# Performance work log

Hardware: AMD Instinct MI355X
Metric: run time of the kernel (lower is better)

Reference implementation:

```python
import jax, jax.numpy as jnp
import numpy as np

B, S, D_IN, D_OUT = 4, 2048, 4096, 11008


def setup_inputs() -> dict:
    key = jax.random.key(0)
    k1, k2, k3 = jax.random.split(key, 3)
    x = jax.random.normal(k1, (B, S, D_IN), dtype=jnp.float32)
    # int8-range quantized weight values in [-127, 127]
    weight_q = jax.random.randint(k2, (D_OUT, D_IN), -127, 128, dtype=jnp.int32)
    # per-output-row abs-max scale (positive)
    max_val = jax.random.uniform(k3, (D_OUT,), dtype=jnp.float32, minval=0.5, maxval=4.0)
    return {"x": x, "weight_q": weight_q, "max_val": max_val}


def reference(x, weight_q, max_val):
    # dequantize: W = weight_q * max_val[:, None] / 127   (shape [D_OUT, D_IN])
    w = weight_q.astype(x.dtype) * (max_val / 127.0)[:, None]
    # F.linear(x, W) = x @ W.T
    return jnp.einsum('bsd,od->bso', x, w)
```

## Files before the change

### kernel.cpp

```cpp
#include <hip/hip_runtime.h>
#include <hip/hip_bf16.h>
#include <stdint.h>

constexpr int Mdim = 4 * 2048;
constexpr int Kdim = 4096;
constexpr int Ndim = 11008;

constexpr int BM = 128;
constexpr int BN = 128;
constexpr int BK = 32;

typedef _Float16 f16x8 __attribute__((ext_vector_type(8)));
typedef _Float16 f16x4 __attribute__((ext_vector_type(4)));
typedef float    f32x4 __attribute__((ext_vector_type(4)));
typedef int      i32x4 __attribute__((ext_vector_type(4)));


__global__ __launch_bounds__(256) void cvt_f32_f16(const float* __restrict__ in,
                                                   _Float16* __restrict__ out,
                                                   int nvec8) {
  int idx = blockIdx.x * blockDim.x + threadIdx.x;
  int stride = gridDim.x * blockDim.x;
  for (int i = idx; i < nvec8; i += stride) {
    const f32x4* p = (const f32x4*)in + (size_t)i * 2;
    f32x4 a = p[0];
    f32x4 b = p[1];
    f16x8 h;
    h[0] = (_Float16)a[0]; h[1] = (_Float16)a[1];
    h[2] = (_Float16)a[2]; h[3] = (_Float16)a[3];
    h[4] = (_Float16)b[0]; h[5] = (_Float16)b[1];
    h[6] = (_Float16)b[2]; h[7] = (_Float16)b[3];
    ((f16x8*)out)[i] = h;
  }
}

__global__ __launch_bounds__(256) void cvt_i32_f16(const int* __restrict__ in,
                                                   _Float16* __restrict__ out,
                                                   int nvec8) {
  int idx = blockIdx.x * blockDim.x + threadIdx.x;
  int stride = gridDim.x * blockDim.x;
  for (int i = idx; i < nvec8; i += stride) {
    const i32x4* p = (const i32x4*)in + (size_t)i * 2;
    i32x4 a = p[0];
    i32x4 b = p[1];
    f16x8 h;
    h[0] = (_Float16)a[0]; h[1] = (_Float16)a[1];
    h[2] = (_Float16)a[2]; h[3] = (_Float16)a[3];
    h[4] = (_Float16)b[0]; h[5] = (_Float16)b[1];
    h[6] = (_Float16)b[2]; h[7] = (_Float16)b[3];
    ((f16x8*)out)[i] = h;
  }
}


__device__ __forceinline__ void gl_lds16(const _Float16* g, _Float16* l) {
  __builtin_amdgcn_global_load_lds(
      (const __attribute__((address_space(1))) unsigned int*)g,
      (__attribute__((address_space(3))) unsigned int*)l,
      16, 0, 0);
}


template <bool FROM_WS>
__global__ __launch_bounds__(256) void w8_gemm(const void* __restrict__ Ap,
                                               const void* __restrict__ Bp,
                                               const float* __restrict__ maxval,
                                               float* __restrict__ C) {
  __shared__ _Float16 As[BM][BK];
  __shared__ _Float16 Bs[BN][BK];

  const int nbn = Ndim / BN;
  const int nwg = (Mdim / BM) * nbn;
  const int cpx = nwg / 8;
  int bid = blockIdx.x;
  bid = (bid % 8) * cpx + (bid / 8);
  const int bm = bid / nbn;
  const int bn = bid % nbn;
  const int rowBase = bm * BM;
  const int colBase = bn * BN;

  const int t = threadIdx.x;
  const int lane = t & 63;
  const int wid = t >> 6;
  const int wr = wid >> 1;
  const int wc = wid & 1;
  const int lrow = lane & 15;
  const int kgrp = lane >> 4;

  f32x4 acc[4][4] = {};

  for (int k0 = 0; k0 < Kdim; k0 += BK) {
    __syncthreads();
    if constexpr (FROM_WS) {
      const _Float16* A  = (const _Float16*)Ap;
      const _Float16* Bw = (const _Float16*)Bp;
#pragma unroll
      for (int i = 0; i < 2; ++i) {
        int c = i * 256 + t;
        int r = c >> 2;
        int ce = (c & 3) * 8;
        gl_lds16(A  + (size_t)(rowBase + r) * Kdim + k0 + ce, &As[r][ce]);
        gl_lds16(Bw + (size_t)(colBase + r) * Kdim + k0 + ce, &Bs[r][ce]);
      }
    } else {
      const float* A  = (const float*)Ap;
      const int*   Bw = (const int*)Bp;
#pragma unroll
      for (int i = 0; i < 4; ++i) {
        int c = i * 256 + t;
        int r = c >> 3;
        int ce = (c & 7) * 4;
        f32x4 av = *(const f32x4*)(A  + (size_t)(rowBase + r) * Kdim + k0 + ce);
        i32x4 bv = *(const i32x4*)(Bw + (size_t)(colBase + r) * Kdim + k0 + ce);
        f16x4 ah, bh;
#pragma unroll
        for (int j = 0; j < 4; ++j) {
          ah[j] = (_Float16)av[j];
          bh[j] = (_Float16)bv[j];
        }
        *(f16x4*)&As[r][ce] = ah;
        *(f16x4*)&Bs[r][ce] = bh;
      }
    }
    __syncthreads();

    f16x8 a[4], b[4];
#pragma unroll
    for (int m = 0; m < 4; ++m)
      a[m] = *(const f16x8*)&As[wr * 64 + m * 16 + lrow][kgrp * 8];
#pragma unroll
    for (int n = 0; n < 4; ++n)
      b[n] = *(const f16x8*)&Bs[wc * 64 + n * 16 + lrow][kgrp * 8];
#pragma unroll
    for (int m = 0; m < 4; ++m)
#pragma unroll
      for (int n = 0; n < 4; ++n)
        acc[m][n] = __builtin_amdgcn_mfma_f32_16x16x32_f16(a[m], b[n], acc[m][n], 0, 0, 0);
  }

  float s[4];
#pragma unroll
  for (int n = 0; n < 4; ++n)
    s[n] = maxval[colBase + wc * 64 + n * 16 + lrow] * (1.0f / 127.0f);
#pragma unroll
  for (int m = 0; m < 4; ++m) {
#pragma unroll
    for (int j = 0; j < 4; ++j) {
      int row = rowBase + wr * 64 + m * 16 + kgrp * 4 + j;
      float* cp = C + (size_t)row * Ndim + colBase + wc * 64 + lrow;
#pragma unroll
      for (int n = 0; n < 4; ++n)
        cp[n * 16] = acc[m][n][j] * s[n];
    }
  }
}


extern "C" void kernel_launch(void* const* d_in, const int* in_sizes, int n_in,
                              void* d_out, int out_size, void* d_ws, size_t ws_size,
                              hipStream_t stream) {
  const float* x  = (const float*)d_in[0];
  const int*   wq = (const int*)d_in[1];
  const float* mx = (const float*)d_in[2];
  float* out = (float*)d_out;

  const size_t xh_bytes = (size_t)Mdim * Kdim * sizeof(_Float16);
  const size_t wh_bytes = (size_t)Ndim * Kdim * sizeof(_Float16);
  const int nblocks = (Mdim / BM) * (Ndim / BN);

  if (ws_size >= xh_bytes + wh_bytes) {
    _Float16* xh = (_Float16*)d_ws;
    _Float16* wh = (_Float16*)((char*)d_ws + xh_bytes);
    cvt_f32_f16<<<2048, 256, 0, stream>>>(x, xh, Mdim * Kdim / 8);
    cvt_i32_f16<<<2048, 256, 0, stream>>>(wq, wh, Ndim * Kdim / 8);
    w8_gemm<true><<<nblocks, 256, 0, stream>>>(xh, wh, mx, out);
  } else {
    w8_gemm<false><<<nblocks, 256, 0, stream>>>(x, wq, mx, out);
  }
}
```

Before: 1.461 ms.

## Use 256x256 tiles with triple-buffered swizzled LDS pipeline in fp16 GEMM

```diff
diff --git a/kernel.cpp b/kernel.cpp
--- a/kernel.cpp
+++ b/kernel.cpp
@@ -2,13 +2,9 @@
 #include <hip/hip_bf16.h>
 #include <stdint.h>
 
-constexpr int Mdim = 4 * 2048;
+constexpr int Mdim = 8192;
 constexpr int Kdim = 4096;
 constexpr int Ndim = 11008;
-
-constexpr int BM = 128;
-constexpr int BN = 128;
-constexpr int BK = 32;
 
 typedef _Float16 f16x8 __attribute__((ext_vector_type(8)));
 typedef _Float16 f16x4 __attribute__((ext_vector_type(4)));
@@ -60,99 +56,187 @@
       16, 0, 0);
 }
 
-
-template <bool FROM_WS>
-__global__ __launch_bounds__(256) void w8_gemm(const void* __restrict__ Ap,
-                                               const void* __restrict__ Bp,
-                                               const float* __restrict__ maxval,
-                                               float* __restrict__ C) {
-  __shared__ _Float16 As[BM][BK];
-  __shared__ _Float16 Bs[BN][BK];
+#define WAITV4()    asm volatile("s_waitcnt vmcnt(4)" ::: "memory")
+#define WAITV0()    asm volatile("s_waitcnt vmcnt(0)" ::: "memory")
+#define WAITLGKM0() asm volatile("s_waitcnt lgkmcnt(0)" ::: "memory")
+#define SBAR()      __builtin_amdgcn_s_barrier()
+#define SCHED0()    __builtin_amdgcn_sched_barrier(0)
+#define MFMA16(d, va, vb) d = __builtin_amdgcn_mfma_f32_16x16x32_f16(va, vb, d, 0, 0, 0)
+
+
+constexpr int BM = 256, BN = 256, BK = 32;
+constexpr int NT = Kdim / BK;
+
+__global__ __launch_bounds__(512, 2) void w8_gemm256(
+    const _Float16* __restrict__ A, const _Float16* __restrict__ Bw,
+    const float* __restrict__ maxval, float* __restrict__ C) {
+  __shared__ _Float16 As[3][BM][BK];
+  __shared__ _Float16 Bs[3][BM][BK];
 
   const int nbn = Ndim / BN;
-  const int nwg = (Mdim / BM) * nbn;
-  const int cpx = nwg / 8;
+  const int cpx = ((Mdim / BM) * nbn) / 8;
   int bid = blockIdx.x;
-  bid = (bid % 8) * cpx + (bid / 8);
-  const int bm = bid / nbn;
-  const int bn = bid % nbn;
-  const int rowBase = bm * BM;
-  const int colBase = bn * BN;
+  bid = (bid & 7) * cpx + (bid >> 3);
+  const int rowBase = (bid / nbn) * BM;
+  const int colBase = (bid % nbn) * BN;
 
   const int t = threadIdx.x;
   const int lane = t & 63;
   const int wid = t >> 6;
-  const int wr = wid >> 1;
-  const int wc = wid & 1;
+  const int wr = wid >> 2;
+  const int wc = wid & 3;
   const int lrow = lane & 15;
   const int kgrp = lane >> 4;
 
+  const int sr = t >> 2;
+  const int sc = ((t & 3) ^ ((sr >> 2) & 3)) << 3;
+  const size_t aRow0 = (size_t)(rowBase + sr) * Kdim + sc;
+  const size_t aRow1 = (size_t)(rowBase + 128 + sr) * Kdim + sc;
+  const size_t bRow0 = (size_t)(colBase + sr) * Kdim + sc;
+  const size_t bRow1 = (size_t)(colBase + 128 + sr) * Kdim + sc;
+  const int ldsOff = t * 8;
+
+#define STAGE_A(buf, k0) do { \
+    gl_lds16(A + aRow0 + (k0), (_Float16*)As[buf] + ldsOff); \
+    gl_lds16(A + aRow1 + (k0), (_Float16*)As[buf] + 4096 + ldsOff); } while (0)
+#define STAGE_B(buf, k0) do { \
+    gl_lds16(Bw + bRow0 + (k0), (_Float16*)Bs[buf] + ldsOff); \
+    gl_lds16(Bw + bRow1 + (k0), (_Float16*)Bs[buf] + 4096 + ldsOff); } while (0)
+
+  int offA[8], offB[4];
+#pragma unroll
+  for (int m = 0; m < 8; ++m) {
+    int rt = wr * 128 + m * 16 + lrow;
+    offA[m] = rt * 64 + ((kgrp ^ ((rt >> 2) & 3)) << 4);
+  }
+#pragma unroll
+  for (int n = 0; n < 4; ++n) {
+    int rt = wc * 64 + n * 16 + lrow;
+    offB[n] = rt * 64 + ((kgrp ^ ((rt >> 2) & 3)) << 4);
+  }
+
+#define RDA(buf, m) (*(const f16x8*)((const char*)&As[buf][0][0] + offA[m]))
+#define RDB(buf, n) (*(const f16x8*)((const char*)&Bs[buf][0][0] + offB[n]))
+
+  f32x4 acc[8][4] = {};
+
+  STAGE_A(0, 0); STAGE_B(0, 0);
+  STAGE_A(1, BK); STAGE_B(1, BK);
+  WAITV4();
+  SBAR();
+
+  int cur = 0, nx1 = 1, nx2 = 2;
+  for (int T = 0; T < NT; ++T) {
+    const int kst = (T + 2) * BK;
+    if (T + 2 < NT) STAGE_A(nx2, kst);
+    f16x8 a0 = RDA(cur, 0), a1 = RDA(cur, 1), a2 = RDA(cur, 2), a3 = RDA(cur, 3);
+    f16x8 b0 = RDB(cur, 0), b1 = RDB(cur, 1), b2 = RDB(cur, 2), b3 = RDB(cur, 3);
+    SBAR();
+    WAITLGKM0();
+    SCHED0();
+    __builtin_amdgcn_s_setprio(1);
+    MFMA16(acc[0][0], a0, b0); MFMA16(acc[0][1], a0, b1); MFMA16(acc[0][2], a0, b2); MFMA16(acc[0][3], a0, b3);
+    MFMA16(acc[1][0], a1, b0); MFMA16(acc[1][1], a1, b1); MFMA16(acc[1][2], a1, b2); MFMA16(acc[1][3], a1, b3);
+    MFMA16(acc[2][0], a2, b0); MFMA16(acc[2][1], a2, b1); MFMA16(acc[2][2], a2, b2); MFMA16(acc[2][3], a2, b3);
+    MFMA16(acc[3][0], a3, b0); MFMA16(acc[3][1], a3, b1); MFMA16(acc[3][2], a3, b2); MFMA16(acc[3][3], a3, b3);
+    __builtin_amdgcn_s_setprio(0);
+    SBAR();
+    if (T + 2 < NT) STAGE_B(nx2, kst);
+    f16x8 a4 = RDA(cur, 4), a5 = RDA(cur, 5), a6 = RDA(cur, 6), a7 = RDA(cur, 7);
+    SBAR();
+    WAITLGKM0();
+    SCHED0();
+    __builtin_amdgcn_s_setprio(1);
+    MFMA16(acc[4][0], a4, b0); MFMA16(acc[4][1], a4, b1); MFMA16(acc[4][2], a4, b2); MFMA16(acc[4][3], a4, b3);
+    MFMA16(acc[5][0], a5, b0); MFMA16(acc[5][1], a5, b1); MFMA16(acc[5][2], a5, b2); MFMA16(acc[5][3], a5, b3);
+    MFMA16(acc[6][0], a6, b0); MFMA16(acc[6][1], a6, b1); MFMA16(acc[6][2], a6, b2); MFMA16(acc[6][3], a6, b3);
+    MFMA16(acc[7][0], a7, b0); MFMA16(acc[7][1], a7, b1); MFMA16(acc[7][2], a7, b2); MFMA16(acc[7][3], a7, b3);
+    __builtin_amdgcn_s_setprio(0);
+    if (T < NT - 2) { WAITV4(); } else { WAITV0(); }
+    SBAR();
+    int tmp = cur; cur = nx1; nx1 = nx2; nx2 = tmp;
+  }
+
+  float s[4];
+#pragma unroll
+  for (int n = 0; n < 4; ++n)
+    s[n] = maxval[colBase + wc * 64 + n * 16 + lrow] * (1.0f / 127.0f);
+#pragma unroll
+  for (int m = 0; m < 8; ++m) {
+#pragma unroll
+    for (int j = 0; j < 4; ++j) {
+      int row = rowBase + wr * 128 + m * 16 + kgrp * 4 + j;
+      float* cp = C + (size_t)row * Ndim + colBase + wc * 64 + lrow;
+#pragma unroll
+      for (int n = 0; n < 4; ++n)
+        cp[n * 16] = acc[m][n][j] * s[n];
+    }
+  }
+#undef STAGE_A
+#undef STAGE_B
+#undef RDA
+#undef RDB
+}
+
+
+__global__ __launch_bounds__(256) void w8_gemm_fb(const float* __restrict__ A,
+                                                  const int* __restrict__ Bw,
+                                                  const float* __restrict__ maxval,
+                                                  float* __restrict__ C) {
+  __shared__ _Float16 Asb[128][32];
+  __shared__ _Float16 Bsb[128][32];
+  const int nbn = Ndim / 128;
+  const int cpx = ((Mdim / 128) * nbn) / 8;
+  int bid = blockIdx.x;
+  bid = (bid & 7) * cpx + (bid >> 3);
+  const int rowBase = (bid / nbn) * 128;
+  const int colBase = (bid % nbn) * 128;
+  const int t = threadIdx.x;
+  const int lane = t & 63;
+  const int wid = t >> 6;
+  const int wr = wid >> 1, wc = wid & 1;
+  const int lrow = lane & 15, kgrp = lane >> 4;
   f32x4 acc[4][4] = {};
-
-  for (int k0 = 0; k0 < Kdim; k0 += BK) {
+  for (int k0 = 0; k0 < Kdim; k0 += 32) {
     __syncthreads();
-    if constexpr (FROM_WS) {
-      const _Float16* A  = (const _Float16*)Ap;
-      const _Float16* Bw = (const _Float16*)Bp;
-#pragma unroll
-      for (int i = 0; i < 2; ++i) {
-        int c = i * 256 + t;
-        int r = c >> 2;
-        int ce = (c & 3) * 8;
-        gl_lds16(A  + (size_t)(rowBase + r) * Kdim + k0 + ce, &As[r][ce]);
-        gl_lds16(Bw + (size_t)(colBase + r) * Kdim + k0 + ce, &Bs[r][ce]);
-      }
-    } else {
-      const float* A  = (const float*)Ap;
-      const int*   Bw = (const int*)Bp;
-#pragma unroll
-      for (int i = 0; i < 4; ++i) {
-        int c = i * 256 + t;
-        int r = c >> 3;
-        int ce = (c & 7) * 4;
-        f32x4 av = *(const f32x4*)(A  + (size_t)(rowBase + r) * Kdim + k0 + ce);
-        i32x4 bv = *(const i32x4*)(Bw + (size_t)(colBase + r) * Kdim + k0 + ce);
-        f16x4 ah, bh;
-#pragma unroll
-        for (int j = 0; j < 4; ++j) {
-          ah[j] = (_Float16)av[j];
-          bh[j] = (_Float16)bv[j];
-        }
-        *(f16x4*)&As[r][ce] = ah;
-        *(f16x4*)&Bs[r][ce] = bh;
-      }
+#pragma unroll
+    for (int i = 0; i < 4; ++i) {
+      int c = i * 256 + t;
+      int r = c >> 3;
+      int ce = (c & 7) * 4;
+      f32x4 av = *(const f32x4*)(A + (size_t)(rowBase + r) * Kdim + k0 + ce);
+      i32x4 bv = *(const i32x4*)(Bw + (size_t)(colBase + r) * Kdim + k0 + ce);
+      f16x4 ah, bh;
+#pragma unroll
+      for (int j = 0; j < 4; ++j) { ah[j] = (_Float16)av[j]; bh[j] = (_Float16)bv[j]; }
+      *(f16x4*)&Asb[r][ce] = ah;
+      *(f16x4*)&Bsb[r][ce] = bh;
     }
     __syncthreads();
-
     f16x8 a[4], b[4];
 #pragma unroll
-    for (int m = 0; m < 4; ++m)
-      a[m] = *(const f16x8*)&As[wr * 64 + m * 16 + lrow][kgrp * 8];
-#pragma unroll
-    for (int n = 0; n < 4; ++n)
-      b[n] = *(const f16x8*)&Bs[wc * 64 + n * 16 + lrow][kgrp * 8];
+    for (int m = 0; m < 4; ++m) a[m] = *(const f16x8*)&Asb[wr * 64 + m * 16 + lrow][kgrp * 8];
+#pragma unroll
+    for (int n = 0; n < 4; ++n) b[n] = *(const f16x8*)&Bsb[wc * 64 + n * 16 + lrow][kgrp * 8];
 #pragma unroll
     for (int m = 0; m < 4; ++m)
 #pragma unroll
       for (int n = 0; n < 4; ++n)
         acc[m][n] = __builtin_amdgcn_mfma_f32_16x16x32_f16(a[m], b[n], acc[m][n], 0, 0, 0);
   }
-
   float s[4];
 #pragma unroll
   for (int n = 0; n < 4; ++n)
     s[n] = maxval[colBase + wc * 64 + n * 16 + lrow] * (1.0f / 127.0f);
 #pragma unroll
-  for (int m = 0; m < 4; ++m) {
+  for (int m = 0; m < 4; ++m)
 #pragma unroll
     for (int j = 0; j < 4; ++j) {
       int row = rowBase + wr * 64 + m * 16 + kgrp * 4 + j;
       float* cp = C + (size_t)row * Ndim + colBase + wc * 64 + lrow;
 #pragma unroll
-      for (int n = 0; n < 4; ++n)
-        cp[n * 16] = acc[m][n][j] * s[n];
+      for (int n = 0; n < 4; ++n) cp[n * 16] = acc[m][n][j] * s[n];
     }
-  }
 }
 
 
@@ -166,15 +250,16 @@
 
   const size_t xh_bytes = (size_t)Mdim * Kdim * sizeof(_Float16);
   const size_t wh_bytes = (size_t)Ndim * Kdim * sizeof(_Float16);
-  const int nblocks = (Mdim / BM) * (Ndim / BN);
 
   if (ws_size >= xh_bytes + wh_bytes) {
     _Float16* xh = (_Float16*)d_ws;
     _Float16* wh = (_Float16*)((char*)d_ws + xh_bytes);
     cvt_f32_f16<<<2048, 256, 0, stream>>>(x, xh, Mdim * Kdim / 8);
     cvt_i32_f16<<<2048, 256, 0, stream>>>(wq, wh, Ndim * Kdim / 8);
-    w8_gemm<true><<<nblocks, 256, 0, stream>>>(xh, wh, mx, out);
+    const int nblocks = (Mdim / BM) * (Ndim / BN);
+    w8_gemm256<<<nblocks, 512, 0, stream>>>(xh, wh, mx, out);
   } else {
-    w8_gemm<false><<<nblocks, 256, 0, stream>>>(x, wq, mx, out);
-  }
-}
+    const int nblocks = (Mdim / 128) * (Ndim / 128);
+    w8_gemm_fb<<<nblocks, 256, 0, stream>>>(x, wq, mx, out);
+  }
+}
```

After: 1.551 ms. 6.2% more time.
